# Performance work log

Hardware: AMD Instinct MI355X
Metric: run time of the kernel (lower is better)

Reference implementation:

```python
import jax, jax.numpy as jnp
import numpy as np
from jax import lax

EPS = 1e-8

def setup_inputs() -> dict:
    key = jax.random.key(0)
    ks = jax.random.split(key, 9)
    B, Cin, H, W = 16, 128, 64, 64
    C = 256
    return {
        "x":  jax.random.normal(ks[0], (B, Cin, H, W), jnp.float32),
        "w1": jax.random.normal(ks[1], (C, Cin, 3, 3), jnp.float32) * 0.02,
        "b1": jax.random.normal(ks[2], (C,), jnp.float32) * 0.02,
        "w2": jax.random.normal(ks[3], (C, C), jnp.float32) * 0.02,
        "b2": jax.random.normal(ks[4], (C,), jnp.float32) * 0.02,
        "w3": jax.random.normal(ks[5], (C, C), jnp.float32) * 0.02,
        "b3": jax.random.normal(ks[6], (C,), jnp.float32) * 0.02,
        "w4": jax.random.normal(ks[7], (C, C), jnp.float32) * 0.02,
        "b4": jax.random.normal(ks[8], (C,), jnp.float32) * 0.02,
    }

def reference(x, w1, b1, w2, b2, w3, b3, w4, b4):
    B = x.shape[0]
    # conv1: 3x3, pad 1 -> [B, 256, H, W]
    conv1 = lax.conv_general_dilated(
        x, w1, window_strides=(1, 1), padding="SAME",
        dimension_numbers=("NCHW", "OIHW", "NCHW")) + b1[None, :, None, None]
    H, W = conv1.shape[2], conv1.shape[3]
    C = conv1.shape[1]
    # gap1 -> [B, 256]; note: forward never applies relu/sigmoid (faithful)
    gap1 = conv1.mean(axis=(2, 3))
    c2 = gap1 @ w2.T + b2            # 1x1 conv on 1x1 spatial == dense
    c3 = c2 @ w3.T + b3              # [B, 256]
    # add1 = conv1 + conv1 * c3 (broadcast scale over spatial)
    add1 = conv1 * (1.0 + c3[:, :, None, None])
    gap2 = add1.mean(axis=(2, 3))    # [B, 256]
    # cosine similarity along channel dim between gap2 and add1 -> [B, H, W]
    num = jnp.einsum("bc,bchw->bhw", gap2, add1)
    n_g = jnp.maximum(jnp.linalg.norm(gap2, axis=1), EPS)[:, None, None]
    n_a = jnp.maximum(jnp.sqrt(jnp.sum(add1 * add1, axis=1)), EPS)
    cos = num / (n_g * n_a)
    r1 = cos.reshape(B, H * W)       # [B, HW]
    m1 = r1.T @ r1                   # [HW, HW] cross-batch position similarity
    # conv4: 1x1 conv -> [B, 256, H, W]
    conv4 = jnp.einsum("oc,bchw->bohw", w4, add1) + b4[None, :, None, None]
    # torch: permute to NHWC then view as [B, 256, HW] (mixes dims; faithful)
    r2 = jnp.transpose(conv4, (0, 2, 3, 1)).reshape(B, C, H * W)
    m2 = r2 @ m1                     # [B, 256, HW]
    return m2.reshape(B, C, H, W)
```

## Files before the change

kernel.cpp:

```cpp
#include <hip/hip_runtime.h>

#define EPSF 1e-8f

typedef __attribute__((ext_vector_type(8))) short bf16x8;
typedef __attribute__((ext_vector_type(16))) float f32x16;

#define MFMA32(a, b, c) __builtin_amdgcn_mfma_f32_32x32x16_bf16(a, b, c, 0, 0, 0)

__device__ __forceinline__ uint32_t splitpack(float v) {
    uint32_t u = __float_as_uint(v);
    uint32_t hb = (u + 0x7fffu + ((u >> 16) & 1u)) & 0xffff0000u;
    float rem = v - __uint_as_float(hb);
    uint32_t r = __float_as_uint(rem);
    uint32_t lb = (r + 0x7fffu + ((r >> 16) & 1u)) >> 16;
    return (hb >> 16) | (lb << 16);
}
__device__ __forceinline__ float unpackf(uint32_t p) {
    return __uint_as_float(p << 16) + __uint_as_float(p & 0xffff0000u);
}

__device__ __forceinline__ void gload_lds16(const void* src, void* dst) {
#if __has_builtin(__builtin_amdgcn_global_load_lds)
    __builtin_amdgcn_global_load_lds(
        (const __attribute__((address_space(1))) uint32_t*)src,
        (__attribute__((address_space(3))) uint32_t*)dst, 16, 0, 0);
#else
    *(uint4*)dst = *(const uint4*)src;
#endif
}

__global__ __launch_bounds__(256) void k_xpack(const float* __restrict__ x,
                                               unsigned short* __restrict__ xph,
                                               unsigned short* __restrict__ xpl) {
    const int bx = blockIdx.x;
    const int hb = bx & 15, cg = (bx >> 4) & 15, b = bx >> 8;
    const int tid = threadIdx.x;
    const int w = tid & 63, hs = tid >> 6;
    const int h = hb * 4 + hs;
    uint32_t hiw[4], low[4];
#pragma unroll
    for (int q = 0; q < 4; ++q) {
        uint32_t u0 = splitpack(x[(((b * 128 + cg * 8 + q * 2) * 64) + h) * 64 + w]);
        uint32_t u1 = splitpack(x[(((b * 128 + cg * 8 + q * 2 + 1) * 64) + h) * 64 + w]);
        hiw[q] = (u0 & 0xffffu) | (u1 << 16);
        low[q] = (u0 >> 16) | (u1 & 0xffff0000u);
    }
    const long o = ((((long)(b * 16 + cg) * 64 + h) * 64) + w) * 8;
    *(uint4*)(xph + o) = *(uint4*)hiw;
    *(uint4*)(xpl + o) = *(uint4*)low;
}

__global__ __launch_bounds__(256) void k_wpack(const float* __restrict__ w1,
                                               short* __restrict__ Bh, short* __restrict__ Bl) {
    int d = blockIdx.x * 256 + threadIdx.x;
    int j = d & 7, lane = (d >> 3) & 63, nt = (d >> 9) & 7, cp = (d >> 12) & 7, tap = d >> 15;
    int oc = nt * 32 + (lane & 31);
    int cin = cp * 16 + (lane >> 5) * 8 + j;
    uint32_t u = splitpack(w1[oc * 1152 + cin * 9 + tap]);
    Bh[d] = (short)(u & 0xffffu);
    Bl[d] = (short)(u >> 16);
}

__global__ __launch_bounds__(512, 4) void k_conv1(
        const unsigned short* __restrict__ xph, const unsigned short* __restrict__ xpl,
        const short* __restrict__ Bh, const short* __restrict__ Bl,
        const float* __restrict__ b1,
        uint32_t* __restrict__ c1p, float* __restrict__ gpart) {
    __shared__ uint4 lds[2 * 2 * 12 * 66];
    const int bx = blockIdx.x;
    const int ot = bx & 3, hp = (bx >> 2) & 15, b = bx >> 6;
    const int h0 = hp * 4;
    const int tid = threadIdx.x;
    const int lane = tid & 63, wv = tid >> 6;
    const int mq = wv >> 1, nh = wv & 1;
    const int l31 = lane & 31, hbit = lane >> 5;

    f32x16 acc[2];
#pragma unroll
    for (int i = 0; i < 2; ++i)
#pragma unroll
        for (int r = 0; r < 16; ++r) acc[i][r] = 0.f;

    auto stage = [&](int buf, int cp) {
#pragma unroll
        for (int i = 0; i < 3; ++i) {
            const int id = wv * 3 + i;
            const int plane = (id >= 12) ? 1 : 0;
            const int u = id - plane * 12;
            const int r6 = u >> 1, kg = u & 1;
            const int grow = h0 - 1 + r6;
            uint4* dst = &lds[((buf * 2 + plane) * 12 + u) * 66 + 1 + lane];
            if ((unsigned)grow < 64u) {
                const unsigned short* pls = plane ? xpl : xph;
                const unsigned short* src =
                    pls + ((((long)(b * 16 + cp * 2 + kg) * 64 + grow) * 64) + lane) * 8;
                gload_lds16(src, dst);
            } else {
                *dst = (uint4){0u, 0u, 0u, 0u};
            }
        }
    };

    stage(0, 0);
    if (tid < 96) {
        const int row = tid >> 1, side = tid & 1;
        lds[row * 66 + (side ? 65 : 0)] = (uint4){0u, 0u, 0u, 0u};
    }
    __syncthreads();

    int buf = 0;
    for (int cp = 0; cp < 8; ++cp) {
        if (cp < 7) stage(buf ^ 1, cp + 1);
        bf16x8 Ah[2][2], Al[2][2], Bhv[2], Blv[2];
#define LOADA(tap, par) do {                                                     \
            const int kh_ = (tap) / 3, kw_ = (tap) % 3;                          \
            _Pragma("unroll")                                                    \
            for (int mt = 0; mt < 2; ++mt) {                                     \
                const int rb = ((buf * 2 + 0) * 12 + (mq + kh_) * 2 + hbit) * 66 \
                               + kw_ + mt * 32 + l31;                            \
                const int rb1 = rb + 12 * 66;                                    \
                Ah[par][mt] = *(const bf16x8*)&lds[rb];                          \
                Al[par][mt] = *(const bf16x8*)&lds[rb1];                         \
            } } while (0)
#define LOADB(tap, par) do {                                                     \
            const int fi = (((tap) * 8 + cp) * 8 + ot * 2 + nh) * 512 + lane * 8; \
            Bhv[par] = *(const bf16x8*)(Bh + fi);                                \
            Blv[par] = *(const bf16x8*)(Bl + fi);                                \
        } while (0)
        LOADA(0, 0); LOADB(0, 0);
#pragma unroll
        for (int tap = 0; tap < 9; ++tap) {
            const int cur = tap & 1, nxt = cur ^ 1;
            if (tap < 8) { LOADA(tap + 1, nxt); LOADB(tap + 1, nxt); }
            __builtin_amdgcn_s_setprio(1);
#pragma unroll
            for (int mt = 0; mt < 2; ++mt) {
                acc[mt] = MFMA32(Ah[cur][mt], Bhv[cur], acc[mt]);
                acc[mt] = MFMA32(Ah[cur][mt], Blv[cur], acc[mt]);
                acc[mt] = MFMA32(Al[cur][mt], Bhv[cur], acc[mt]);
            }
            __builtin_amdgcn_s_setprio(0);
        }
#undef LOADA
#undef LOADB
        __syncthreads();
        buf ^= 1;
    }

    const int hrow = h0 + mq;
    const int oc = ot * 64 + nh * 32 + l31;
    {
        float g = 0.f;
#pragma unroll
        for (int mt = 0; mt < 2; ++mt)
#pragma unroll
            for (int r = 0; r < 16; ++r) g += acc[mt][r];
        g += __shfl_xor(g, 32);
        if (hbit == 0) gpart[((b * 16 + hp) * 4 + mq) * 256 + oc] = g;
    }
    const float bias = b1[oc];
#pragma unroll
    for (int mt = 0; mt < 2; ++mt) {
#pragma unroll
        for (int r = 0; r < 16; ++r) {
            const int row = (r & 3) + 8 * (r >> 2) + 4 * hbit;
            const int p = hrow * 64 + mt * 32 + row;
            c1p[((long)(b * 4096 + p)) * 256 + oc] = splitpack(acc[mt][r] + bias);
        }
    }
}

__global__ __launch_bounds__(256) void k_mlp(const float* __restrict__ gpart,
                                             const float* __restrict__ b1,
                                             const float* __restrict__ w2, const float* __restrict__ b2,
                                             const float* __restrict__ w3, const float* __restrict__ b3,
                                             float* __restrict__ scale, float* __restrict__ ga,
                                             float* __restrict__ n_g) {
    int b = blockIdx.x, tid = threadIdx.x;
    __shared__ float gs[256], c2s[256], red[4];
    float g = 0.f;
#pragma unroll 8
    for (int i = 0; i < 64; ++i) g += gpart[(b * 64 + i) * 256 + tid];
    gs[tid] = g * (1.f / 4096.f) + b1[tid];
    __syncthreads();
    {
        const float4* wr = (const float4*)(w2 + tid * 256);
        float a = b2[tid];
#pragma unroll 8
        for (int c4 = 0; c4 < 64; c4++) {
            float4 wv = wr[c4];
            a += wv.x * gs[c4*4] + wv.y * gs[c4*4+1] + wv.z * gs[c4*4+2] + wv.w * gs[c4*4+3];
        }
        c2s[tid] = a;
    }
    __syncthreads();
    float a3 = b3[tid];
    {
        const float4* wr = (const float4*)(w3 + tid * 256);
#pragma unroll 8
        for (int c4 = 0; c4 < 64; c4++) {
            float4 wv = wr[c4];
            a3 += wv.x * c2s[c4*4] + wv.y * c2s[c4*4+1] + wv.z * c2s[c4*4+2] + wv.w * c2s[c4*4+3];
        }
    }
    float s1 = 1.f + a3;
    float g2 = gs[tid] * s1;
    scale[b * 256 + tid] = s1;
    ga[b * 256 + tid] = g2 * s1;
    float r = g2 * g2;
    for (int off = 32; off; off >>= 1) r += __shfl_down(r, off);
    if ((tid & 63) == 0) red[tid >> 6] = r;
    __syncthreads();
    if (tid == 0) n_g[b] = fmaxf(sqrtf(red[0] + red[1] + red[2] + red[3]), EPSF);
}

__global__ __launch_bounds__(256) void k_cos(
        const uint32_t* __restrict__ c1p,
        const float* __restrict__ scale, const float* __restrict__ ga,
        const float* __restrict__ n_g, float* __restrict__ r1) {
    const int bx = blockIdx.x;
    const int pt = bx & 63, b = bx >> 6;
    const int tid = threadIdx.x;
    const int lane = tid & 63, wv = tid >> 6;
    const int half = lane >> 5, l31 = lane & 31;
    float ga8[8], sc8[8];
#pragma unroll
    for (int q = 0; q < 8; ++q) {
        ga8[q] = ga[b * 256 + l31 * 8 + q];
        sc8[q] = scale[b * 256 + l31 * 8 + q];
    }
    const float ng = n_g[b];
#pragma unroll
    for (int pp = 0; pp < 8; ++pp) {
        const int p = pt * 64 + wv * 16 + pp * 2 + half;
        const uint32_t* base = c1p + ((long)(b * 4096 + p)) * 256 + l31 * 8;
        uint4 a = *(const uint4*)base;
        uint4 bq = *(const uint4*)(base + 4);
        uint32_t pk[8] = {a.x, a.y, a.z, a.w, bq.x, bq.y, bq.z, bq.w};
        float num = 0.f, den = 0.f;
#pragma unroll
        for (int q = 0; q < 8; ++q) {
            const float v = unpackf(pk[q]);
            num += ga8[q] * v;
            const float t = sc8[q] * v;
            den += t * t;
        }
#pragma unroll
        for (int off = 1; off <= 16; off <<= 1) {
            num += __shfl_xor(num, off);
            den += __shfl_xor(den, off);
        }
        if (l31 == 0) {
            float na = fmaxf(sqrtf(den), EPSF);
            r1[b * 4096 + p] = num / (ng * na);
        }
    }
}

__global__ __launch_bounds__(256) void k_u(const float* __restrict__ r1,
                                           const float* __restrict__ w4,
                                           const float* __restrict__ b4,
                                           float* __restrict__ Uf, float* __restrict__ Dpart) {
    const int g = blockIdx.x;
    const int tid = threadIdx.x;
    __shared__ float rs[256], red[4];
    rs[tid] = r1[(g >> 4) * 4096 + (g & 15) * 256 + tid];
    __syncthreads();
    float a = 0.f;
#pragma unroll 8
    for (int o = 0; o < 256; ++o) a += rs[o] * w4[o * 256 + tid];
    Uf[(g >> 4) * 4096 + (g & 15) * 256 + tid] = a;
    float d = b4[tid] * rs[tid];
    for (int off = 32; off; off >>= 1) d += __shfl_down(d, off);
    if ((tid & 63) == 0) red[tid >> 6] = d;
    __syncthreads();
    if (tid == 0) Dpart[g] = red[0] + red[1] + red[2] + red[3];
}

__global__ __launch_bounds__(256) void k_t2(const uint32_t* __restrict__ c1p,
                                            const float* __restrict__ Uf,
                                            const float* __restrict__ scale,
                                            const float* __restrict__ Dpart,
                                            float* __restrict__ tmat) {
    __shared__ float Ac[16][256];
    __shared__ float Bc[16][260];
    __shared__ float scs[256];
    const int bx = blockIdx.x;
    const int b = bx >> 4, it = bx & 15;
    const int tid = threadIdx.x;
    const int il = tid >> 4, bp = tid & 15;
    scs[tid] = scale[b * 256 + tid];
    float acc = 0.f;
    for (int jc = 0; jc < 16; ++jc) {
        __syncthreads();
#pragma unroll
        for (int q = 0; q < 4; ++q) {
            const int f4i = tid + q * 256;
            const int row = f4i >> 6, col4 = f4i & 63;
            uint4 u = *(const uint4*)(c1p +
                ((long)(b * 4096 + it * 256 + row * 16 + jc)) * 256 + col4 * 4);
            Ac[row][col4 * 4 + 0] = unpackf(u.x) * scs[col4 * 4 + 0];
            Ac[row][col4 * 4 + 1] = unpackf(u.y) * scs[col4 * 4 + 1];
            Ac[row][col4 * 4 + 2] = unpackf(u.z) * scs[col4 * 4 + 2];
            Ac[row][col4 * 4 + 3] = unpackf(u.w) * scs[col4 * 4 + 3];
            *(float4*)&Bc[row][col4 * 4] =
                *(const float4*)(Uf + (long)row * 4096 + jc * 256 + col4 * 4);
        }
        __syncthreads();
#pragma unroll 8
        for (int j = 0; j < 256; j += 4) {
            float4 a4  = *(const float4*)&Ac[il][j];
            float4 b4v = *(const float4*)&Bc[bp][j];
            acc += a4.x * b4v.x + a4.y * b4v.y + a4.z * b4v.z + a4.w * b4v.w;
        }
    }
    float D = 0.f;
#pragma unroll
    for (int pr = 0; pr < 16; ++pr) D += Dpart[bp * 16 + pr];
    tmat[((b * 256) + it * 16 + il) * 16 + bp] = acc + D;
}

__global__ __launch_bounds__(256) void k_m2(const float* __restrict__ tmat,
                                            const float* __restrict__ r1,
                                            float* __restrict__ outb) {
    __shared__ float r1s[16][512];
    __shared__ float ts[256];
    int bx = blockIdx.x;
    int b = bx >> 7, it = (bx >> 3) & 15, pc = bx & 7;
    int tid = threadIdx.x;
    ts[tid] = tmat[(b * 256 + it * 16) * 16 + tid];
#pragma unroll
    for (int k = 0; k < 8; k++) {
        int f4i = tid + k * 256;
        int row = f4i >> 7, col = f4i & 127;
        *(float4*)&r1s[row][col * 4] = *(const float4*)(r1 + ((long)row << 12) + pc * 512 + col * 4);
    }
    __syncthreads();
    for (int il = 0; il < 16; il++) {
        float tv[16];
#pragma unroll
        for (int bp = 0; bp < 16; bp++) tv[bp] = ts[il * 16 + bp];
#pragma unroll
        for (int k = 0; k < 2; k++) {
            int p = k * 256 + tid;
            float s = 0.f;
#pragma unroll
            for (int bp = 0; bp < 16; bp++) s += tv[bp] * r1s[bp][p];
            outb[((long)b << 20) + ((long)(it * 16 + il) << 12) + pc * 512 + p] = s;
        }
    }
}

extern "C" void kernel_launch(void* const* d_in, const int* in_sizes, int n_in,
                              void* d_out, int out_size, void* d_ws, size_t ws_size,
                              hipStream_t stream) {
    const float* x  = (const float*)d_in[0];
    const float* w1 = (const float*)d_in[1];
    const float* b1 = (const float*)d_in[2];
    const float* w2 = (const float*)d_in[3];
    const float* b2 = (const float*)d_in[4];
    const float* w3 = (const float*)d_in[5];
    const float* b3 = (const float*)d_in[6];
    const float* w4 = (const float*)d_in[7];
    const float* b4 = (const float*)d_in[8];
    float* out = (float*)d_out;

    unsigned short* xph = (unsigned short*)d_out;
    unsigned short* xpl = xph + 8388608L;

    char* p = (char*)d_ws;
    uint32_t* c1p = (uint32_t*)p;  p += 16777216L * 4;
    short* Bh  = (short*)p;  p += 294912L * 2;
    short* Bl  = (short*)p;  p += 294912L * 2;
    float* gpart = (float*)p; p += 262144L * 4;
    float* scale = (float*)p; p += 4096L * 4;
    float* ga    = (float*)p; p += 4096L * 4;
    float* n_g   = (float*)p; p += 16L * 4;
    float* r1    = (float*)p; p += 65536L * 4;
    float* tmat  = (float*)p; p += 65536L * 4;
    float* Uf    = (float*)p; p += 65536L * 4;
    float* Dpart = (float*)p; p += 256L * 4;

    k_xpack <<<4096, 256, 0, stream>>>(x, xph, xpl);
    k_wpack <<<1152, 256, 0, stream>>>(w1, Bh, Bl);
    k_conv1 <<<1024, 512, 0, stream>>>(xph, xpl, Bh, Bl, b1, c1p, gpart);
    k_mlp   <<<16,   256, 0, stream>>>(gpart, b1, w2, b2, w3, b3, scale, ga, n_g);
    k_cos   <<<1024, 256, 0, stream>>>(c1p, scale, ga, n_g, r1);
    k_u     <<<256,  256, 0, stream>>>(r1, w4, b4, Uf, Dpart);
    k_t2    <<<256,  256, 0, stream>>>(c1p, Uf, scale, Dpart, tmat);
    k_m2    <<<2048, 256, 0, stream>>>(tmat, r1, out);
}
```

Baseline: 243.7 us.

## Retile conv1 onto 16x16x32 MFMA with swizzled LDS and wider K chunks

Rewrites the conv1 implicit-GEMM kernel to use 16x16x32 bf16 MFMAs. Each wave now computes a 64-pixel by 64-channel tile as a 4x4 set of accumulators, using 256-thread blocks that cover 2 rows by 128 output channels. The staged input now holds 32 input channels per step in an XOR-swizzled LDS layout to avoid bank conflicts, and the weight pre-pack is reordered to match. The aim is more operand reuse per LDS and global load. In exchange, the double-buffered staging is replaced by a single buffer with two barriers per K step, so loads no longer overlap compute.

```diff
diff --git a/kernel.cpp b/kernel.cpp
--- a/kernel.cpp
+++ b/kernel.cpp
@@ -3,9 +3,9 @@
 #define EPSF 1e-8f
 
 typedef __attribute__((ext_vector_type(8))) short bf16x8;
-typedef __attribute__((ext_vector_type(16))) float f32x16;
-
-#define MFMA32(a, b, c) __builtin_amdgcn_mfma_f32_32x32x16_bf16(a, b, c, 0, 0, 0)
+typedef __attribute__((ext_vector_type(4))) float f32x4;
+
+#define MFMA16(a, b, c) __builtin_amdgcn_mfma_f32_16x16x32_bf16(a, b, c, 0, 0, 0)
 
 __device__ __forceinline__ uint32_t splitpack(float v) {
     uint32_t u = __float_as_uint(v);
@@ -53,120 +53,123 @@
 __global__ __launch_bounds__(256) void k_wpack(const float* __restrict__ w1,
                                                short* __restrict__ Bh, short* __restrict__ Bl) {
     int d = blockIdx.x * 256 + threadIdx.x;
-    int j = d & 7, lane = (d >> 3) & 63, nt = (d >> 9) & 7, cp = (d >> 12) & 7, tap = d >> 15;
-    int oc = nt * 32 + (lane & 31);
-    int cin = cp * 16 + (lane >> 5) * 8 + j;
+    int j = d & 7, lane = (d >> 3) & 63, nt = (d >> 9) & 15, cp = (d >> 13) & 3, tap = d >> 15;
+    int oc = nt * 16 + (lane & 15);
+    int cin = cp * 32 + (lane >> 4) * 8 + j;
     uint32_t u = splitpack(w1[oc * 1152 + cin * 9 + tap]);
     Bh[d] = (short)(u & 0xffffu);
     Bl[d] = (short)(u >> 16);
 }
 
-__global__ __launch_bounds__(512, 4) void k_conv1(
+__global__ __launch_bounds__(256, 4) void k_conv1(
         const unsigned short* __restrict__ xph, const unsigned short* __restrict__ xpl,
         const short* __restrict__ Bh, const short* __restrict__ Bl,
         const float* __restrict__ b1,
         uint32_t* __restrict__ c1p, float* __restrict__ gpart) {
-    __shared__ uint4 lds[2 * 2 * 12 * 66];
+    __shared__ short lds[2 * 4 * 66 * 32];
     const int bx = blockIdx.x;
-    const int ot = bx & 3, hp = (bx >> 2) & 15, b = bx >> 6;
-    const int h0 = hp * 4;
+    const int ot = bx & 1, hp = (bx >> 1) & 31, b = bx >> 6;
+    const int h0 = hp * 2;
     const int tid = threadIdx.x;
     const int lane = tid & 63, wv = tid >> 6;
-    const int mq = wv >> 1, nh = wv & 1;
-    const int l31 = lane & 31, hbit = lane >> 5;
-
-    f32x16 acc[2];
-#pragma unroll
-    for (int i = 0; i < 2; ++i)
-#pragma unroll
-        for (int r = 0; r < 16; ++r) acc[i][r] = 0.f;
-
-    auto stage = [&](int buf, int cp) {
-#pragma unroll
-        for (int i = 0; i < 3; ++i) {
-            const int id = wv * 3 + i;
-            const int plane = (id >= 12) ? 1 : 0;
-            const int u = id - plane * 12;
-            const int r6 = u >> 1, kg = u & 1;
-            const int grow = h0 - 1 + r6;
-            uint4* dst = &lds[((buf * 2 + plane) * 12 + u) * 66 + 1 + lane];
+    const int pw = wv >> 1, ow = wv & 1;
+    const int l15 = lane & 15, kq = lane >> 4;
+
+    f32x4 acc[4][4];
+#pragma unroll
+    for (int i = 0; i < 4; ++i)
+#pragma unroll
+        for (int j = 0; j < 4; ++j) acc[i][j] = (f32x4){0.f, 0.f, 0.f, 0.f};
+
+    auto stage = [&](int cp) {
+#pragma unroll
+        for (int i = 0; i < 8; ++i) {
+            const int pl = wv >> 1;
+            const int r  = ((wv & 1) << 1) | (i >> 2);
+            const int wl = 1 + (i & 3) * 16 + (lane >> 2);
+            const int chg = lane & 3;
+            const int grow = h0 - 1 + r;
+            short* dst = &lds[(((pl * 4 + r) * 66 + wl) * 32) + chg * 8];
             if ((unsigned)grow < 64u) {
-                const unsigned short* pls = plane ? xpl : xph;
+                const unsigned short* pls = pl ? xpl : xph;
+                const int chs = chg ^ ((wl >> 1) & 3);
                 const unsigned short* src =
-                    pls + ((((long)(b * 16 + cp * 2 + kg) * 64 + grow) * 64) + lane) * 8;
+                    pls + ((((long)(b * 16 + cp * 4 + chs) * 64 + grow) * 64) + (wl - 1)) * 8;
                 gload_lds16(src, dst);
             } else {
-                *dst = (uint4){0u, 0u, 0u, 0u};
+                *(uint4*)dst = (uint4){0u, 0u, 0u, 0u};
             }
         }
     };
 
-    stage(0, 0);
-    if (tid < 96) {
-        const int row = tid >> 1, side = tid & 1;
-        lds[row * 66 + (side ? 65 : 0)] = (uint4){0u, 0u, 0u, 0u};
-    }
-    __syncthreads();
-
-    int buf = 0;
-    for (int cp = 0; cp < 8; ++cp) {
-        if (cp < 7) stage(buf ^ 1, cp + 1);
-        bf16x8 Ah[2][2], Al[2][2], Bhv[2], Blv[2];
-#define LOADA(tap, par) do {                                                     \
-            const int kh_ = (tap) / 3, kw_ = (tap) % 3;                          \
-            _Pragma("unroll")                                                    \
-            for (int mt = 0; mt < 2; ++mt) {                                     \
-                const int rb = ((buf * 2 + 0) * 12 + (mq + kh_) * 2 + hbit) * 66 \
-                               + kw_ + mt * 32 + l31;                            \
-                const int rb1 = rb + 12 * 66;                                    \
-                Ah[par][mt] = *(const bf16x8*)&lds[rb];                          \
-                Al[par][mt] = *(const bf16x8*)&lds[rb1];                         \
-            } } while (0)
-#define LOADB(tap, par) do {                                                     \
-            const int fi = (((tap) * 8 + cp) * 8 + ot * 2 + nh) * 512 + lane * 8; \
-            Bhv[par] = *(const bf16x8*)(Bh + fi);                                \
-            Blv[par] = *(const bf16x8*)(Bl + fi);                                \
-        } while (0)
-        LOADA(0, 0); LOADB(0, 0);
-#pragma unroll
-        for (int tap = 0; tap < 9; ++tap) {
-            const int cur = tap & 1, nxt = cur ^ 1;
-            if (tap < 8) { LOADA(tap + 1, nxt); LOADB(tap + 1, nxt); }
-            __builtin_amdgcn_s_setprio(1);
-#pragma unroll
-            for (int mt = 0; mt < 2; ++mt) {
-                acc[mt] = MFMA32(Ah[cur][mt], Bhv[cur], acc[mt]);
-                acc[mt] = MFMA32(Ah[cur][mt], Blv[cur], acc[mt]);
-                acc[mt] = MFMA32(Al[cur][mt], Bhv[cur], acc[mt]);
+    stage(0);
+    if (tid < 64) {
+        const int side = tid & 1, chq = (tid >> 1) & 3, r = (tid >> 3) & 3, pl = tid >> 5;
+        *(uint4*)&lds[(((pl * 4 + r) * 66 + (side ? 65 : 0)) * 32) + chq * 8] =
+            (uint4){0u, 0u, 0u, 0u};
+    }
+    __syncthreads();
+
+    for (int cp = 0; cp < 4; ++cp) {
+#pragma unroll
+        for (int kh = 0; kh < 3; ++kh) {
+            const int r = pw + kh;
+#pragma unroll
+            for (int kw = 0; kw < 3; ++kw) {
+                bf16x8 ah[4], al[4];
+#pragma unroll
+                for (int mt = 0; mt < 4; ++mt) {
+                    const int wl = mt * 16 + l15 + kw;
+                    const int ch0 = (kq ^ ((wl >> 1) & 3)) * 8;
+                    ah[mt] = *(const bf16x8*)&lds[((0 + r) * 66 + wl) * 32 + ch0];
+                    al[mt] = *(const bf16x8*)&lds[((4 + r) * 66 + wl) * 32 + ch0];
+                }
+                const int tap = kh * 3 + kw;
+#pragma unroll
+                for (int nt = 0; nt < 4; ++nt) {
+                    const int ntg = ot * 8 + ow * 4 + nt;
+                    const long fi = (long)(((tap * 4 + cp) * 16 + ntg) * 512) + lane * 8;
+                    const bf16x8 bh = *(const bf16x8*)(Bh + fi);
+                    const bf16x8 bl = *(const bf16x8*)(Bl + fi);
+                    __builtin_amdgcn_s_setprio(1);
+#pragma unroll
+                    for (int mt = 0; mt < 4; ++mt) {
+                        acc[mt][nt] = MFMA16(ah[mt], bh, acc[mt][nt]);
+                        acc[mt][nt] = MFMA16(ah[mt], bl, acc[mt][nt]);
+                        acc[mt][nt] = MFMA16(al[mt], bh, acc[mt][nt]);
+                    }
+                    __builtin_amdgcn_s_setprio(0);
+                }
             }
-            __builtin_amdgcn_s_setprio(0);
-        }
-#undef LOADA
-#undef LOADB
-        __syncthreads();
-        buf ^= 1;
-    }
-
-    const int hrow = h0 + mq;
-    const int oc = ot * 64 + nh * 32 + l31;
-    {
+        }
+        if (cp < 3) {
+            __syncthreads();
+            stage(cp + 1);
+            __syncthreads();
+        }
+    }
+
+    const int h = h0 + pw;
+#pragma unroll
+    for (int nt = 0; nt < 4; ++nt) {
+        const int oc = ot * 128 + ow * 64 + nt * 16 + l15;
         float g = 0.f;
 #pragma unroll
-        for (int mt = 0; mt < 2; ++mt)
-#pragma unroll
-            for (int r = 0; r < 16; ++r) g += acc[mt][r];
+        for (int mt = 0; mt < 4; ++mt)
+#pragma unroll
+            for (int rg = 0; rg < 4; ++rg) g += acc[mt][nt][rg];
+        g += __shfl_xor(g, 16);
         g += __shfl_xor(g, 32);
-        if (hbit == 0) gpart[((b * 16 + hp) * 4 + mq) * 256 + oc] = g;
-    }
-    const float bias = b1[oc];
-#pragma unroll
-    for (int mt = 0; mt < 2; ++mt) {
-#pragma unroll
-        for (int r = 0; r < 16; ++r) {
-            const int row = (r & 3) + 8 * (r >> 2) + 4 * hbit;
-            const int p = hrow * 64 + mt * 32 + row;
-            c1p[((long)(b * 4096 + p)) * 256 + oc] = splitpack(acc[mt][r] + bias);
-        }
+        if (kq == 0) gpart[((b * 32 + hp) * 2 + pw) * 256 + oc] = g;
+        const float bias = b1[oc];
+#pragma unroll
+        for (int mt = 0; mt < 4; ++mt)
+#pragma unroll
+            for (int rg = 0; rg < 4; ++rg) {
+                const int w = mt * 16 + kq * 4 + rg;
+                c1p[((long)(b * 4096 + h * 64 + w)) * 256 + oc] =
+                    splitpack(acc[mt][nt][rg] + bias);
+            }
     }
 }
 
@@ -383,7 +386,7 @@
 
     k_xpack <<<4096, 256, 0, stream>>>(x, xph, xpl);
     k_wpack <<<1152, 256, 0, stream>>>(w1, Bh, Bl);
-    k_conv1 <<<1024, 512, 0, stream>>>(xph, xpl, Bh, Bl, b1, c1p, gpart);
+    k_conv1 <<<1024, 256, 0, stream>>>(xph, xpl, Bh, Bl, b1, c1p, gpart);
     k_mlp   <<<16,   256, 0, stream>>>(gpart, b1, w2, b2, w3, b3, scale, ga, n_g);
     k_cos   <<<1024, 256, 0, stream>>>(c1p, scale, ga, n_g, r1);
     k_u     <<<256,  256, 0, stream>>>(r1, w4, b4, Uf, Dpart);
```

Measured after the change: 476.5 us. 1.96x slower.

## Widen conv1 output-channel tile per wave and use nontemporal loads/stores

Applied to the files above, without the earlier changes.

Each conv1 block now covers 128 output channels instead of 64, so each wave computes two N tiles and reuses the LDS-loaded A fragments across both. This halves the grid and halves redundant staging of input rows into LDS. The A fragments are loaded per tap instead of being prefetched. Global-to-LDS loads and the c1p stores are marked nontemporal. The cost is doubled accumulator registers, which may reduce occupancy under launch_bounds(512,4).

```diff
diff --git a/kernel.cpp b/kernel.cpp
--- a/kernel.cpp
+++ b/kernel.cpp
@@ -19,11 +19,11 @@
     return __uint_as_float(p << 16) + __uint_as_float(p & 0xffff0000u);
 }
 
-__device__ __forceinline__ void gload_lds16(const void* src, void* dst) {
+__device__ __forceinline__ void gload_lds16nt(const void* src, void* dst) {
 #if __has_builtin(__builtin_amdgcn_global_load_lds)
     __builtin_amdgcn_global_load_lds(
         (const __attribute__((address_space(1))) uint32_t*)src,
-        (__attribute__((address_space(3))) uint32_t*)dst, 16, 0, 0);
+        (__attribute__((address_space(3))) uint32_t*)dst, 16, 0, 2);
 #else
     *(uint4*)dst = *(const uint4*)src;
 #endif
@@ -68,18 +68,20 @@
         uint32_t* __restrict__ c1p, float* __restrict__ gpart) {
     __shared__ uint4 lds[2 * 2 * 12 * 66];
     const int bx = blockIdx.x;
-    const int ot = bx & 3, hp = (bx >> 2) & 15, b = bx >> 6;
+    const int ot = bx & 1, hp = (bx >> 1) & 15, b = bx >> 5;
     const int h0 = hp * 4;
     const int tid = threadIdx.x;
     const int lane = tid & 63, wv = tid >> 6;
     const int mq = wv >> 1, nh = wv & 1;
     const int l31 = lane & 31, hbit = lane >> 5;
 
-    f32x16 acc[2];
+    f32x16 acc[2][2];
 #pragma unroll
     for (int i = 0; i < 2; ++i)
 #pragma unroll
-        for (int r = 0; r < 16; ++r) acc[i][r] = 0.f;
+        for (int j = 0; j < 2; ++j)
+#pragma unroll
+            for (int r = 0; r < 16; ++r) acc[i][j][r] = 0.f;
 
     auto stage = [&](int buf, int cp) {
 #pragma unroll
@@ -94,7 +96,7 @@
                 const unsigned short* pls = plane ? xpl : xph;
                 const unsigned short* src =
                     pls + ((((long)(b * 16 + cp * 2 + kg) * 64 + grow) * 64) + lane) * 8;
-                gload_lds16(src, dst);
+                gload_lds16nt(src, dst);
             } else {
                 *dst = (uint4){0u, 0u, 0u, 0u};
             }
@@ -111,61 +113,65 @@
     int buf = 0;
     for (int cp = 0; cp < 8; ++cp) {
         if (cp < 7) stage(buf ^ 1, cp + 1);
-        bf16x8 Ah[2][2], Al[2][2], Bhv[2], Blv[2];
-#define LOADA(tap, par) do {                                                     \
-            const int kh_ = (tap) / 3, kw_ = (tap) % 3;                          \
-            _Pragma("unroll")                                                    \
-            for (int mt = 0; mt < 2; ++mt) {                                     \
-                const int rb = ((buf * 2 + 0) * 12 + (mq + kh_) * 2 + hbit) * 66 \
-                               + kw_ + mt * 32 + l31;                            \
-                const int rb1 = rb + 12 * 66;                                    \
-                Ah[par][mt] = *(const bf16x8*)&lds[rb];                          \
-                Al[par][mt] = *(const bf16x8*)&lds[rb1];                         \
+        bf16x8 Bhv[2][2], Blv[2][2];
+#define LOADB(tap, par) do {                                                      \
+            _Pragma("unroll")                                                     \
+            for (int nt = 0; nt < 2; ++nt) {                                      \
+                const int fi = (((tap) * 8 + cp) * 8 + ot * 4 + nh * 2 + nt) * 512 + lane * 8; \
+                Bhv[par][nt] = *(const bf16x8*)(Bh + fi);                         \
+                Blv[par][nt] = *(const bf16x8*)(Bl + fi);                         \
             } } while (0)
-#define LOADB(tap, par) do {                                                     \
-            const int fi = (((tap) * 8 + cp) * 8 + ot * 2 + nh) * 512 + lane * 8; \
-            Bhv[par] = *(const bf16x8*)(Bh + fi);                                \
-            Blv[par] = *(const bf16x8*)(Bl + fi);                                \
-        } while (0)
-        LOADA(0, 0); LOADB(0, 0);
+        LOADB(0, 0);
 #pragma unroll
         for (int tap = 0; tap < 9; ++tap) {
             const int cur = tap & 1, nxt = cur ^ 1;
-            if (tap < 8) { LOADA(tap + 1, nxt); LOADB(tap + 1, nxt); }
+            if (tap < 8) LOADB(tap + 1, nxt);
+            const int kh = tap / 3, kw = tap % 3;
+            bf16x8 ah[2], al[2];
+#pragma unroll
+            for (int mt = 0; mt < 2; ++mt) {
+                const int rb = ((buf * 2 + 0) * 12 + (mq + kh) * 2 + hbit) * 66
+                               + kw + mt * 32 + l31;
+                ah[mt] = *(const bf16x8*)&lds[rb];
+                al[mt] = *(const bf16x8*)&lds[rb + 12 * 66];
+            }
             __builtin_amdgcn_s_setprio(1);
 #pragma unroll
-            for (int mt = 0; mt < 2; ++mt) {
-                acc[mt] = MFMA32(Ah[cur][mt], Bhv[cur], acc[mt]);
-                acc[mt] = MFMA32(Ah[cur][mt], Blv[cur], acc[mt]);
-                acc[mt] = MFMA32(Al[cur][mt], Bhv[cur], acc[mt]);
-            }
+            for (int nt = 0; nt < 2; ++nt)
+#pragma unroll
+                for (int mt = 0; mt < 2; ++mt) {
+                    acc[mt][nt] = MFMA32(ah[mt], Bhv[cur][nt], acc[mt][nt]);
+                    acc[mt][nt] = MFMA32(ah[mt], Blv[cur][nt], acc[mt][nt]);
+                    acc[mt][nt] = MFMA32(al[mt], Bhv[cur][nt], acc[mt][nt]);
+                }
             __builtin_amdgcn_s_setprio(0);
         }
-#undef LOADA
 #undef LOADB
         __syncthreads();
         buf ^= 1;
     }
 
     const int hrow = h0 + mq;
-    const int oc = ot * 64 + nh * 32 + l31;
-    {
+#pragma unroll
+    for (int nt = 0; nt < 2; ++nt) {
+        const int oc = ot * 128 + (nh * 2 + nt) * 32 + l31;
         float g = 0.f;
 #pragma unroll
         for (int mt = 0; mt < 2; ++mt)
 #pragma unroll
-            for (int r = 0; r < 16; ++r) g += acc[mt][r];
+            for (int r = 0; r < 16; ++r) g += acc[mt][nt][r];
         g += __shfl_xor(g, 32);
         if (hbit == 0) gpart[((b * 16 + hp) * 4 + mq) * 256 + oc] = g;
-    }
-    const float bias = b1[oc];
-#pragma unroll
-    for (int mt = 0; mt < 2; ++mt) {
-#pragma unroll
-        for (int r = 0; r < 16; ++r) {
-            const int row = (r & 3) + 8 * (r >> 2) + 4 * hbit;
-            const int p = hrow * 64 + mt * 32 + row;
-            c1p[((long)(b * 4096 + p)) * 256 + oc] = splitpack(acc[mt][r] + bias);
+        const float bias = b1[oc];
+#pragma unroll
+        for (int mt = 0; mt < 2; ++mt) {
+#pragma unroll
+            for (int r = 0; r < 16; ++r) {
+                const int row = (r & 3) + 8 * (r >> 2) + 4 * hbit;
+                const int p = hrow * 64 + mt * 32 + row;
+                __builtin_nontemporal_store(splitpack(acc[mt][nt][r] + bias),
+                                            &c1p[((long)(b * 4096 + p)) * 256 + oc]);
+            }
         }
     }
 }
@@ -383,7 +389,7 @@
 
     k_xpack <<<4096, 256, 0, stream>>>(x, xph, xpl);
     k_wpack <<<1152, 256, 0, stream>>>(w1, Bh, Bl);
-    k_conv1 <<<1024, 512, 0, stream>>>(xph, xpl, Bh, Bl, b1, c1p, gpart);
+    k_conv1 <<<512,  512, 0, stream>>>(xph, xpl, Bh, Bl, b1, c1p, gpart);
     k_mlp   <<<16,   256, 0, stream>>>(gpart, b1, w2, b2, w3, b3, scale, ga, n_g);
     k_cos   <<<1024, 256, 0, stream>>>(c1p, scale, ga, n_g, r1);
     k_u     <<<256,  256, 0, stream>>>(r1, w4, b4, Uf, Dpart);
```

New measurement: 259.9 us. 6.6% more time.
